# Optimization experiments

Hardware: AMD Instinct MI355X
Metric: run time of the kernel (lower is better)

## Reference

```python
import jax, jax.numpy as jnp
import numpy as np

NUM_QUERIES = 900
EMBED_DIM = 256
NUM_HEADS = 8
EPS = 1e-5


def bilinear_sample(feats, grid):
    """F.grid_sample(..., align_corners=False, padding_mode='zeros', bilinear).
    feats: [BN, C, H, W], grid: [BN, Q, 2] in [-1,1] (x, y). Returns [BN, Q, C]."""
    BN, C, H, W = feats.shape
    ix = (grid[..., 0] + 1.0) * (W * 0.5) - 0.5
    iy = (grid[..., 1] + 1.0) * (H * 0.5) - 0.5
    x0 = jnp.floor(ix)
    y0 = jnp.floor(iy)
    wx1 = ix - x0
    wy1 = iy - y0
    x0i = x0.astype(jnp.int32)
    y0i = y0.astype(jnp.int32)
    x1i = x0i + 1
    y1i = y0i + 1
    b = jnp.arange(BN)[:, None]

    def gather(yy, xx):
        inb = (xx >= 0) & (xx < W) & (yy >= 0) & (yy < H)
        yc = jnp.clip(yy, 0, H - 1)
        xc = jnp.clip(xx, 0, W - 1)
        v = feats[b, :, yc, xc]  # [BN, Q, C]
        return v * inb[..., None].astype(feats.dtype)

    out = (gather(y0i, x0i) * ((1 - wx1) * (1 - wy1))[..., None]
           + gather(y0i, x1i) * (wx1 * (1 - wy1))[..., None]
           + gather(y1i, x0i) * ((1 - wx1) * wy1)[..., None]
           + gather(y1i, x1i) * (wx1 * wy1)[..., None])
    return out


def setup_inputs() -> dict:
    key = jax.random.key(0)
    ks = jax.random.split(key, 16)
    B, N, C, H, W = 2, 6, 256, 116, 200
    Q, D = NUM_QUERIES, EMBED_DIM
    s = 0.02
    return {
        "image_features": jax.random.normal(ks[0], (B, N, C, H, W), jnp.float32),
        "lidar2img": jax.random.normal(ks[1], (B, N, 4, 4), jnp.float32),
        "query_embedding": jax.random.normal(ks[2], (Q, D), jnp.float32) * s,
        "ref_w": jax.random.normal(ks[3], (3, D), jnp.float32) * s,
        "ref_b": jnp.zeros((3,), jnp.float32),
        "in_proj_w": jax.random.normal(ks[4], (3 * D, D), jnp.float32) * s,
        "in_proj_b": jnp.zeros((3 * D,), jnp.float32),
        "out_proj_w": jax.random.normal(ks[5], (D, D), jnp.float32) * s,
        "out_proj_b": jnp.zeros((D,), jnp.float32),
        "norm_w": jnp.ones((D,), jnp.float32),
        "norm_b": jnp.zeros((D,), jnp.float32),
        "cls_w": jax.random.normal(ks[6], (2, D), jnp.float32) * s,
        "cls_b": jnp.zeros((2,), jnp.float32),
        "box_w": jax.random.normal(ks[7], (6, D), jnp.float32) * s,
        "box_b": jnp.zeros((6,), jnp.float32),
    }


def reference(image_features, lidar2img, query_embedding, ref_w, ref_b,
              in_proj_w, in_proj_b, out_proj_w, out_proj_b,
              norm_w, norm_b, cls_w, cls_b, box_w, box_b):
    B, N, C, H, W = image_features.shape
    Q, D = query_embedding.shape

    q = jnp.broadcast_to(query_embedding[None], (B, Q, D))

    # reference points in [0,1]^3
    ref = jax.nn.sigmoid(q @ ref_w.T + ref_b)  # [B,Q,3]

    # 3D -> 2D projection per camera
    homo = jnp.concatenate([ref, jnp.ones_like(ref[..., :1])], axis=-1)  # [B,Q,4]
    p2h = jnp.einsum('bnij,bqj->bnqi', lidar2img, homo)  # [B,N,Q,4]
    z = p2h[..., 2:3]
    pts2d = p2h[..., 0:2] / (jnp.abs(z) + 1e-5)  # [B,N,Q,2]
    mask = (z > 1e-5)[..., 0]  # [B,N,Q]

    # normalize to [-1,1]
    pn = jnp.stack([pts2d[..., 0] / (W - 1) * 2 - 1,
                    pts2d[..., 1] / (H - 1) * 2 - 1], axis=-1)  # [B,N,Q,2]

    feats_flat = image_features.reshape(B * N, C, H, W)
    grid = pn.reshape(B * N, Q, 2)
    sampled = bilinear_sample(feats_flat, grid)            # [BN,Q,C]
    sampled = sampled.reshape(B, N, Q, C).transpose(0, 2, 1, 3)  # [B,Q,N,C]

    mask_t = mask.transpose(0, 2, 1)[..., None]  # [B,Q,N,1]
    # faithful to torch .view(B,Q,N,2): a raw row-major reshape, not a transpose
    pn_view = pn.reshape(B, Q, N, 2)
    valid = mask_t & (jnp.max(jnp.abs(pn_view), axis=-1, keepdims=True) < 1)  # [B,Q,N,1]
    validf = valid.astype(sampled.dtype)

    sum_feats = jnp.sum(sampled * validf, axis=2)  # [B,Q,C]
    count = jnp.clip(jnp.sum(validf, axis=2), 1.0, None)
    tgt = sum_feats / count

    x = q + tgt  # [B,Q,D]

    # MultiheadAttention (batch_first, 8 heads, no dropout)
    qkv = x @ in_proj_w.T + in_proj_b
    qh, kh, vh = jnp.split(qkv, 3, axis=-1)
    hd = D // NUM_HEADS
    def heads(t):
        return t.reshape(B, Q, NUM_HEADS, hd).transpose(0, 2, 1, 3)  # [B,h,Q,hd]
    qh, kh, vh = heads(qh), heads(kh), heads(vh)
    scores = jnp.einsum('bhqd,bhkd->bhqk', qh, kh) / jnp.sqrt(jnp.asarray(hd, x.dtype))
    attn = jax.nn.softmax(scores, axis=-1)
    o = jnp.einsum('bhqk,bhkd->bhqd', attn, vh).transpose(0, 2, 1, 3).reshape(B, Q, D)
    o = o @ out_proj_w.T + out_proj_b

    # LayerNorm (no residual, faithful to the module)
    mu = jnp.mean(o, axis=-1, keepdims=True)
    var = jnp.mean((o - mu) ** 2, axis=-1, keepdims=True)
    xn = (o - mu) / jnp.sqrt(var + EPS) * norm_w + norm_b

    box = xn @ box_w.T + box_b
    box = jnp.concatenate([jax.nn.sigmoid(box[..., :3]), box[..., 3:]], axis=-1)
    cls = xn @ cls_w.T + cls_b
    return cls, box
```

## Files before the change

kernel.cpp:

```cpp
#include <hip/hip_runtime.h>
#include <math.h>

#define BB 2
#define NCAM 6
#define CC 256
#define HH 116
#define WW 200
#define QQ 900
#define DD 256
#define NHD 8
#define HD 32
#define HWSZ (HH*WW)

__device__ __forceinline__ float sigmoidf_(float x){ return 1.0f/(1.0f+expf(-x)); }

__global__ void ref_kernel(const float* __restrict__ qe, const float* __restrict__ ref_w,
                           const float* __restrict__ ref_b, float* __restrict__ ref) {
    int idx = blockIdx.x*256 + threadIdx.x;
    if (idx >= QQ*3) return;
    int q = idx/3, j = idx%3;
    float acc = ref_b[j];
    const float4* qr = (const float4*)(qe + q*DD);
    const float4* wr = (const float4*)(ref_w + j*DD);
    for (int k=0;k<DD/4;k++) {
        float4 a = qr[k], w = wr[k];
        acc += a.x*w.x + a.y*w.y + a.z*w.z + a.w*w.w;
    }
    ref[idx] = sigmoidf_(acc);
}

__global__ void proj_kernel(const float* __restrict__ l2i, const float* __restrict__ ref,
        float* __restrict__ wxa, float* __restrict__ wya,
        int* __restrict__ x0a, int* __restrict__ y0a,
        int* __restrict__ maskz, int* __restrict__ inimg) {
    int idx = blockIdx.x*256+threadIdx.x;
    if (idx >= BB*NCAM*QQ) return;
    int q = idx % QQ;
    int bn = idx / QQ;
    float h0 = ref[q*3+0], h1 = ref[q*3+1], h2 = ref[q*3+2];
    const float* m = l2i + bn*16;
    float px = m[0]*h0+m[1]*h1+m[2]*h2+m[3];
    float py = m[4]*h0+m[5]*h1+m[6]*h2+m[7];
    float pz = m[8]*h0+m[9]*h1+m[10]*h2+m[11];
    float denom = fabsf(pz)+1e-5f;
    float sx = px/denom, sy = py/denom;
    float pnx = sx/(float)(WW-1)*2.0f-1.0f;
    float pny = sy/(float)(HH-1)*2.0f-1.0f;
    maskz[idx] = (pz > 1e-5f) ? 1 : 0;
    inimg[idx] = (fmaxf(fabsf(pnx),fabsf(pny)) < 1.0f) ? 1 : 0;
    float ix = (pnx+1.0f)*(WW*0.5f)-0.5f;
    float iy = (pny+1.0f)*(HH*0.5f)-0.5f;
    float x0f = floorf(ix), y0f = floorf(iy);
    wxa[idx] = ix-x0f; wya[idx] = iy-y0f;
    x0a[idx] = (int)x0f; y0a[idx] = (int)y0f;
}

__global__ __launch_bounds__(256) void sample_kernel(const float* __restrict__ feats,
        const float* __restrict__ qe, const float* __restrict__ wxa, const float* __restrict__ wya,
        const int* __restrict__ x0a, const int* __restrict__ y0a,
        const int* __restrict__ maskz, const int* __restrict__ inimg,
        float* __restrict__ xout) {
    int bq = blockIdx.x;
    int b = bq / QQ, q = bq % QQ;
    int c = threadIdx.x;
    float sum = 0.0f;
    int cnt = 0;
    #pragma unroll
    for (int n = 0; n < NCAM; n++) {
        int s = (b*NCAM+n)*QQ + q;
        int sq = b*(NCAM*QQ) + q*NCAM + n;
        int v = maskz[s] & inimg[sq];
        if (!v) continue;
        cnt++;
        float wx = wxa[s], wy = wya[s];
        int x0 = x0a[s], y0 = y0a[s];
        int x1 = x0 + 1, y1 = y0 + 1;
        bool x0in = (unsigned)x0 < (unsigned)WW;
        bool x1in = (unsigned)x1 < (unsigned)WW;
        bool y0in = (unsigned)y0 < (unsigned)HH;
        bool y1in = (unsigned)y1 < (unsigned)HH;
        int x0c = x0in ? x0 : 0;
        int x1c = x1in ? x1 : (WW-1);
        int y0c = y0in ? y0 : 0;
        int y1c = y1in ? y1 : (HH-1);
        float w00 = (x0in && y0in) ? (1.f-wx)*(1.f-wy) : 0.f;
        float w10 = (x1in && y0in) ? wx*(1.f-wy) : 0.f;
        float w01 = (x0in && y1in) ? (1.f-wx)*wy : 0.f;
        float w11 = (x1in && y1in) ? wx*wy : 0.f;
        const float* fb = feats + ((size_t)(b*NCAM+n)*CC + c)*HWSZ;
        const float* r0 = fb + y0c*WW;
        const float* r1 = fb + y1c*WW;
        sum += w00*r0[x0c] + w10*r0[x1c] + w01*r1[x0c] + w11*r1[x1c];
    }
    float tgt = sum / (float)(cnt > 0 ? cnt : 1);
    xout[(size_t)bq*DD + c] = qe[q*DD+c] + tgt;
}

#define TILE 64
#define BKK 16
__global__ __launch_bounds__(256) void sgemm_nt(const float* __restrict__ A,
        const float* __restrict__ Bw, const float* __restrict__ bias,
        float* __restrict__ Cm, int M, int N, int K) {
    __shared__ float As[BKK][TILE+4];
    __shared__ float Bs[BKK][TILE+4];
    int tid = threadIdx.x;
    int m0 = blockIdx.y * TILE, n0 = blockIdx.x * TILE;
    float acc[4][4] = {};
    int tx = tid & 15, ty = tid >> 4;
    int ms = tid >> 2;
    int kq = (tid & 3) * 4;
    for (int k0 = 0; k0 < K; k0 += BKK) {
        int gm = m0 + ms;
        float4 fa = (gm < M) ? *(const float4*)(A + (size_t)gm * K + k0 + kq)
                             : make_float4(0.f,0.f,0.f,0.f);
        As[kq+0][ms]=fa.x; As[kq+1][ms]=fa.y; As[kq+2][ms]=fa.z; As[kq+3][ms]=fa.w;
        int gn = n0 + ms;
        float4 fb = (gn < N) ? *(const float4*)(Bw + (size_t)gn * K + k0 + kq)
                             : make_float4(0.f,0.f,0.f,0.f);
        Bs[kq+0][ms]=fb.x; Bs[kq+1][ms]=fb.y; Bs[kq+2][ms]=fb.z; Bs[kq+3][ms]=fb.w;
        __syncthreads();
        #pragma unroll
        for (int k = 0; k < BKK; k++) {
            float a[4], bb[4];
            #pragma unroll
            for (int i = 0; i < 4; i++) a[i] = As[k][ty*4+i];
            #pragma unroll
            for (int j = 0; j < 4; j++) bb[j] = Bs[k][tx*4+j];
            #pragma unroll
            for (int i = 0; i < 4; i++)
                #pragma unroll
                for (int j = 0; j < 4; j++)
                    acc[i][j] += a[i] * bb[j];
        }
        __syncthreads();
    }
    for (int i = 0; i < 4; i++) {
        int gm = m0 + ty*4 + i;
        if (gm >= M) continue;
        for (int j = 0; j < 4; j++) {
            int gn = n0 + tx*4 + j;
            if (gn < N) Cm[(size_t)gm * N + gn] = acc[i][j] + bias[gn];
        }
    }
}

#define QTILE 32
#define KTILE 64
#define NQB 29
__global__ __launch_bounds__(256) void attn_flash(const float* __restrict__ qkv,
        float* __restrict__ opA, float* __restrict__ opB,
        float* __restrict__ lpA, float* __restrict__ lpB) {
    __shared__ __align__(16) float Ks[32][68];
    __shared__ __align__(16) float Vs[64][36];
    __shared__ __align__(16) float Ps[32][68];
    int blk = blockIdx.x;
    int qb = blk % NQB;
    int h  = (blk / NQB) % NHD;
    int b  = (blk / (NQB*NHD)) % BB;
    int ks = blk / (NQB*NHD*BB);
    int q0 = qb * QTILE;
    int tid = threadIdx.x;
    int tx = tid & 15, ty = tid >> 4;

    {
        int q = tid >> 3;
        int dseg = (tid & 7) * 4;
        int gq = q0 + q; if (gq > QQ-1) gq = QQ-1;
        const float4 f = *(const float4*)(qkv + ((size_t)(b*QQ+gq))*768 + h*HD + dseg);
        Ps[dseg+0][q] = f.x; Ps[dseg+1][q] = f.y; Ps[dseg+2][q] = f.z; Ps[dseg+3][q] = f.w;
    }
    __syncthreads();
    float q0r[32], q1r[32];
    #pragma unroll
    for (int d = 0; d < 32; d++) { q0r[d] = Ps[d][ty*2]; q1r[d] = Ps[d][ty*2+1]; }
    __syncthreads();

    float O[2][2] = {};
    float l[2] = {0.f, 0.f};
    const float scale = 0.17677669529663689f;
    int kt0 = ks ? 8 : 0;
    int kt1 = ks ? 15 : 8;

    for (int kt = kt0; kt < kt1; kt++) {
        int k0 = kt * KTILE;
        {
            int k = tid >> 2;
            int dseg = (tid & 3) * 8;
            int gk = k0 + k; if (gk > QQ-1) gk = QQ-1;
            const float* kp = qkv + ((size_t)(b*QQ+gk))*768 + 256 + h*HD + dseg;
            float4 f0 = *(const float4*)(kp);
            float4 f1 = *(const float4*)(kp+4);
            Ks[dseg+0][k]=f0.x; Ks[dseg+1][k]=f0.y; Ks[dseg+2][k]=f0.z; Ks[dseg+3][k]=f0.w;
            Ks[dseg+4][k]=f1.x; Ks[dseg+5][k]=f1.y; Ks[dseg+6][k]=f1.z; Ks[dseg+7][k]=f1.w;
            const float* vp = qkv + ((size_t)(b*QQ+gk))*768 + 512 + h*HD + dseg;
            *(float4*)(&Vs[k][dseg])   = *(const float4*)(vp);
            *(float4*)(&Vs[k][dseg+4]) = *(const float4*)(vp+4);
        }
        __syncthreads();

        float acc[2][4] = {};
        #pragma unroll
        for (int d = 0; d < 32; d++) {
            float4 bk = *(const float4*)(&Ks[d][tx*4]);
            float a0 = q0r[d], a1 = q1r[d];
            acc[0][0] += a0*bk.x; acc[0][1] += a0*bk.y; acc[0][2] += a0*bk.z; acc[0][3] += a0*bk.w;
            acc[1][0] += a1*bk.x; acc[1][1] += a1*bk.y; acc[1][2] += a1*bk.z; acc[1][3] += a1*bk.w;
        }
        #pragma unroll
        for (int i = 0; i < 2; i++) {
            float e[4];
            float rs = 0.f;
            #pragma unroll
            for (int j = 0; j < 4; j++) {
                int gk = k0 + tx*4 + j;
                float v = (gk < QQ) ? __expf(acc[i][j]*scale) : 0.f;
                e[j] = v; rs += v;
            }
            #pragma unroll
            for (int m = 1; m < 16; m <<= 1) rs += __shfl_xor(rs, m, 16);
            l[i] += rs;
            *(float4*)(&Ps[ty*2+i][tx*4]) = make_float4(e[0],e[1],e[2],e[3]);
        }
        __syncthreads();

        #pragma unroll
        for (int k4 = 0; k4 < 16; k4++) {
            float4 p0 = *(const float4*)(&Ps[ty*2][k4*4]);
            float4 p1 = *(const float4*)(&Ps[ty*2+1][k4*4]);
            float2 v0 = *(const float2*)(&Vs[k4*4+0][tx*2]);
            float2 v1 = *(const float2*)(&Vs[k4*4+1][tx*2]);
            float2 v2 = *(const float2*)(&Vs[k4*4+2][tx*2]);
            float2 v3 = *(const float2*)(&Vs[k4*4+3][tx*2]);
            O[0][0] += p0.x*v0.x + p0.y*v1.x + p0.z*v2.x + p0.w*v3.x;
            O[0][1] += p0.x*v0.y + p0.y*v1.y + p0.z*v2.y + p0.w*v3.y;
            O[1][0] += p1.x*v0.x + p1.y*v1.x + p1.z*v2.x + p1.w*v3.x;
            O[1][1] += p1.x*v0.y + p1.y*v1.y + p1.z*v2.y + p1.w*v3.y;
        }
        __syncthreads();
    }

    float* op = ks ? opB : opA;
    float* lp = ks ? lpB : lpA;
    #pragma unroll
    for (int i = 0; i < 2; i++) {
        int gq = q0 + ty*2 + i;
        if (gq < QQ) {
            float* o = op + (((size_t)(b*NHD+h))*QQ + gq)*HD + tx*2;
            o[0] = O[i][0];
            o[1] = O[i][1];
            if (tx == 0) lp[(b*NHD+h)*QQ + gq] = l[i];
        }
    }
}

__global__ __launch_bounds__(256) void attn_combine(const float* __restrict__ opA,
        const float* __restrict__ opB, const float* __restrict__ lpA,
        const float* __restrict__ lpB, float* __restrict__ attn_out) {
    int idx = blockIdx.x*256 + threadIdx.x;
    if (idx >= BB*QQ*DD) return;
    int c = idx & 255;
    int bq = idx >> 8;
    int b = bq / QQ, q = bq % QQ;
    int h = c >> 5, d = c & 31;
    size_t base = ((size_t)(b*NHD+h))*QQ + q;
    float o = opA[base*HD + d] + opB[base*HD + d];
    float L = lpA[base] + lpB[base];
    attn_out[idx] = o / L;
}

__global__ __launch_bounds__(256) void final_kernel(const float* __restrict__ o,
    const float* __restrict__ norm_w, const float* __restrict__ norm_b,
    const float* __restrict__ cls_w, const float* __restrict__ cls_b,
    const float* __restrict__ box_w, const float* __restrict__ box_b,
    float* __restrict__ out) {
    __shared__ float s_xn[DD];
    __shared__ float red[8];
    int bq = blockIdx.x;
    int t = threadIdx.x;
    float val = o[(size_t)bq*DD + t];
    float v1 = val, v2 = val*val;
    for (int off=32; off>0; off>>=1) { v1 += __shfl_down(v1, off); v2 += __shfl_down(v2, off); }
    if ((t & 63) == 0) { red[t>>6] = v1; red[4 + (t>>6)] = v2; }
    __syncthreads();
    float ssum = red[0]+red[1]+red[2]+red[3];
    float ssq  = red[4]+red[5]+red[6]+red[7];
    float mu = ssum / (float)DD;
    float var = ssq / (float)DD - mu*mu;
    float inv = 1.0f / sqrtf(var + 1e-5f);
    s_xn[t] = (val - mu)*inv*norm_w[t] + norm_b[t];
    __syncthreads();
    int j = t >> 5, lane = t & 31;
    const float* wrow = (j < 2) ? (cls_w + j*DD) : (box_w + (j-2)*DD);
    float acc = 0.f;
    for (int k=lane; k<DD; k+=32) acc += s_xn[k]*wrow[k];
    for (int off=16; off>0; off>>=1) acc += __shfl_down(acc, off, 32);
    if (lane == 0) {
        if (j < 2) {
            out[(size_t)bq*2 + j] = acc + cls_b[j];
        } else {
            int jj = j-2;
            float v = acc + box_b[jj];
            if (jj < 3) v = sigmoidf_(v);
            out[BB*QQ*2 + (size_t)bq*6 + jj] = v;
        }
    }
}

extern "C" void kernel_launch(void* const* d_in, const int* in_sizes, int n_in,
                              void* d_out, int out_size, void* d_ws, size_t ws_size,
                              hipStream_t stream) {
    const float* feats = (const float*)d_in[0];
    const float* l2i   = (const float*)d_in[1];
    const float* qe    = (const float*)d_in[2];
    const float* ref_w = (const float*)d_in[3];
    const float* ref_b = (const float*)d_in[4];
    const float* ipw   = (const float*)d_in[5];
    const float* ipb   = (const float*)d_in[6];
    const float* opw   = (const float*)d_in[7];
    const float* opb   = (const float*)d_in[8];
    const float* nw    = (const float*)d_in[9];
    const float* nb    = (const float*)d_in[10];
    const float* clsw  = (const float*)d_in[11];
    const float* clsb  = (const float*)d_in[12];
    const float* boxw  = (const float*)d_in[13];
    const float* boxb  = (const float*)d_in[14];
    float* out = (float*)d_out;
    float* ws = (float*)d_ws;

    float* ref   = ws;
    float* wxa   = ws + 2700;
    float* wya   = wxa + 10800;
    int*   x0a   = (int*)(wya + 10800);
    int*   y0a   = x0a + 10800;
    int*   maskz = y0a + 10800;
    int*   inimg = maskz + 10800;
    float* x     = (float*)(inimg + 10800);
    float* qkv   = x + 460800;
    float* attn  = qkv + 1382400;
    float* oproj = attn + 460800;

    float* opA = x;
    float* opB = oproj;
    float* lpA = wxa;
    float* lpB = wxa + 14400;

    ref_kernel<<<(QQ*3+255)/256, 256, 0, stream>>>(qe, ref_w, ref_b, ref);
    proj_kernel<<<(BB*NCAM*QQ+255)/256, 256, 0, stream>>>(l2i, ref, wxa, wya, x0a, y0a, maskz, inimg);
    sample_kernel<<<BB*QQ, 256, 0, stream>>>(feats, qe, wxa, wya, x0a, y0a, maskz, inimg, x);
    sgemm_nt<<<dim3(768/TILE, (BB*QQ+TILE-1)/TILE), 256, 0, stream>>>(x, ipw, ipb, qkv, BB*QQ, 768, 256);
    attn_flash<<<BB*NHD*NQB*2, 256, 0, stream>>>(qkv, opA, opB, lpA, lpB);
    attn_combine<<<(BB*QQ*DD+255)/256, 256, 0, stream>>>(opA, opB, lpA, lpB, attn);
    sgemm_nt<<<dim3(256/TILE, (BB*QQ+TILE-1)/TILE), 256, 0, stream>>>(attn, opw, opb, oproj, BB*QQ, 256, 256);
    final_kernel<<<BB*QQ, 256, 0, stream>>>(oproj, nw, nb, clsw, clsb, boxw, boxb, out);
}
```

Before: 469.7 us.

## Fuse ref projection into proj, batch sampler loads, fold attn combine into GEMM

The ref-point linear plus sigmoid is computed inside proj_kernel, so ref_kernel is gone. sample_kernel stages the per-camera sampling parameters in shared memory and issues all bilinear gathers before reducing, which exposes more memory-level parallelism. The split-K attention combine (sum the partials and divide by L) is folded into the output-projection GEMM's A-tile load, removing a kernel launch and an intermediate buffer round trip. The cost is redundant ref dot products (once per camera and batch) and a heavier A-load path in the GEMM.

```diff
diff --git a/kernel.cpp b/kernel.cpp
--- a/kernel.cpp
+++ b/kernel.cpp
@@ -14,22 +14,8 @@
 
 __device__ __forceinline__ float sigmoidf_(float x){ return 1.0f/(1.0f+expf(-x)); }
 
-__global__ void ref_kernel(const float* __restrict__ qe, const float* __restrict__ ref_w,
-                           const float* __restrict__ ref_b, float* __restrict__ ref) {
-    int idx = blockIdx.x*256 + threadIdx.x;
-    if (idx >= QQ*3) return;
-    int q = idx/3, j = idx%3;
-    float acc = ref_b[j];
-    const float4* qr = (const float4*)(qe + q*DD);
-    const float4* wr = (const float4*)(ref_w + j*DD);
-    for (int k=0;k<DD/4;k++) {
-        float4 a = qr[k], w = wr[k];
-        acc += a.x*w.x + a.y*w.y + a.z*w.z + a.w*w.w;
-    }
-    ref[idx] = sigmoidf_(acc);
-}
-
-__global__ void proj_kernel(const float* __restrict__ l2i, const float* __restrict__ ref,
+__global__ void proj_kernel(const float* __restrict__ l2i, const float* __restrict__ qe,
+        const float* __restrict__ ref_w, const float* __restrict__ ref_b,
         float* __restrict__ wxa, float* __restrict__ wya,
         int* __restrict__ x0a, int* __restrict__ y0a,
         int* __restrict__ maskz, int* __restrict__ inimg) {
@@ -37,7 +23,20 @@
     if (idx >= BB*NCAM*QQ) return;
     int q = idx % QQ;
     int bn = idx / QQ;
-    float h0 = ref[q*3+0], h1 = ref[q*3+1], h2 = ref[q*3+2];
+    float a0 = ref_b[0], a1 = ref_b[1], a2 = ref_b[2];
+    const float4* qr = (const float4*)(qe + (size_t)q*DD);
+    const float4* w0 = (const float4*)(ref_w);
+    const float4* w1 = (const float4*)(ref_w + DD);
+    const float4* w2 = (const float4*)(ref_w + 2*DD);
+    #pragma unroll 4
+    for (int k=0;k<DD/4;k++) {
+        float4 a = qr[k];
+        float4 b0 = w0[k], b1 = w1[k], b2 = w2[k];
+        a0 += a.x*b0.x + a.y*b0.y + a.z*b0.z + a.w*b0.w;
+        a1 += a.x*b1.x + a.y*b1.y + a.z*b1.z + a.w*b1.w;
+        a2 += a.x*b2.x + a.y*b2.y + a.z*b2.z + a.w*b2.w;
+    }
+    float h0 = sigmoidf_(a0), h1 = sigmoidf_(a1), h2 = sigmoidf_(a2);
     const float* m = l2i + bn*16;
     float px = m[0]*h0+m[1]*h1+m[2]*h2+m[3];
     float py = m[4]*h0+m[5]*h1+m[6]*h2+m[7];
@@ -60,20 +59,29 @@
         const int* __restrict__ x0a, const int* __restrict__ y0a,
         const int* __restrict__ maskz, const int* __restrict__ inimg,
         float* __restrict__ xout) {
+    __shared__ float swx[NCAM], swy[NCAM];
+    __shared__ int sx0[NCAM], sy0[NCAM], sval[NCAM];
     int bq = blockIdx.x;
     int b = bq / QQ, q = bq % QQ;
-    int c = threadIdx.x;
-    float sum = 0.0f;
+    int t = threadIdx.x;
+    if (t < NCAM) {
+        int n = t;
+        int s = (b*NCAM+n)*QQ + q;
+        int sq = b*(NCAM*QQ) + q*NCAM + n;
+        sval[n] = maskz[s] & inimg[sq];
+        swx[n] = wxa[s]; swy[n] = wya[s];
+        sx0[n] = x0a[s]; sy0[n] = y0a[s];
+    }
+    __syncthreads();
+    int c = t;
+    float v00[NCAM] = {}, v10[NCAM] = {}, v01[NCAM] = {}, v11[NCAM] = {};
+    float W00[NCAM], W10[NCAM], W01[NCAM], W11[NCAM];
     int cnt = 0;
     #pragma unroll
     for (int n = 0; n < NCAM; n++) {
-        int s = (b*NCAM+n)*QQ + q;
-        int sq = b*(NCAM*QQ) + q*NCAM + n;
-        int v = maskz[s] & inimg[sq];
-        if (!v) continue;
-        cnt++;
-        float wx = wxa[s], wy = wya[s];
-        int x0 = x0a[s], y0 = y0a[s];
+        int valid = sval[n];
+        float wx = swx[n], wy = swy[n];
+        int x0 = sx0[n], y0 = sy0[n];
         int x1 = x0 + 1, y1 = y0 + 1;
         bool x0in = (unsigned)x0 < (unsigned)WW;
         bool x1in = (unsigned)x1 < (unsigned)WW;
@@ -83,22 +91,32 @@
         int x1c = x1in ? x1 : (WW-1);
         int y0c = y0in ? y0 : 0;
         int y1c = y1in ? y1 : (HH-1);
-        float w00 = (x0in && y0in) ? (1.f-wx)*(1.f-wy) : 0.f;
-        float w10 = (x1in && y0in) ? wx*(1.f-wy) : 0.f;
-        float w01 = (x0in && y1in) ? (1.f-wx)*wy : 0.f;
-        float w11 = (x1in && y1in) ? wx*wy : 0.f;
-        const float* fb = feats + ((size_t)(b*NCAM+n)*CC + c)*HWSZ;
-        const float* r0 = fb + y0c*WW;
-        const float* r1 = fb + y1c*WW;
-        sum += w00*r0[x0c] + w10*r0[x1c] + w01*r1[x0c] + w11*r1[x1c];
-    }
+        W00[n] = (x0in && y0in) ? (1.f-wx)*(1.f-wy) : 0.f;
+        W10[n] = (x1in && y0in) ? wx*(1.f-wy) : 0.f;
+        W01[n] = (x0in && y1in) ? (1.f-wx)*wy : 0.f;
+        W11[n] = (x1in && y1in) ? wx*wy : 0.f;
+        cnt += valid;
+        if (valid) {
+            const float* fb = feats + ((size_t)(b*NCAM+n)*CC + c)*HWSZ;
+            const float* r0 = fb + y0c*WW;
+            const float* r1 = fb + y1c*WW;
+            v00[n] = r0[x0c]; v10[n] = r0[x1c];
+            v01[n] = r1[x0c]; v11[n] = r1[x1c];
+        }
+    }
+    float sum = 0.0f;
+    #pragma unroll
+    for (int n = 0; n < NCAM; n++)
+        sum += W00[n]*v00[n] + W10[n]*v10[n] + W01[n]*v01[n] + W11[n]*v11[n];
     float tgt = sum / (float)(cnt > 0 ? cnt : 1);
     xout[(size_t)bq*DD + c] = qe[q*DD+c] + tgt;
 }
 
 #define TILE 64
 #define BKK 16
+template<bool COMB>
 __global__ __launch_bounds__(256) void sgemm_nt(const float* __restrict__ A,
+        const float* __restrict__ A2, const float* __restrict__ lA, const float* __restrict__ lB,
         const float* __restrict__ Bw, const float* __restrict__ bias,
         float* __restrict__ Cm, int M, int N, int K) {
     __shared__ float As[BKK][TILE+4];
@@ -111,8 +129,23 @@
     int kq = (tid & 3) * 4;
     for (int k0 = 0; k0 < K; k0 += BKK) {
         int gm = m0 + ms;
-        float4 fa = (gm < M) ? *(const float4*)(A + (size_t)gm * K + k0 + kq)
-                             : make_float4(0.f,0.f,0.f,0.f);
+        float4 fa = make_float4(0.f,0.f,0.f,0.f);
+        if (gm < M) {
+            if (COMB) {
+                int k = k0 + kq;
+                int h = k >> 5, d = k & 31;
+                int b = (gm >= QQ) ? 1 : 0;
+                int qq_ = gm - b*QQ;
+                size_t base = ((size_t)(b*NHD+h))*QQ + qq_;
+                const float4 o1 = *(const float4*)(A  + base*HD + d);
+                const float4 o2 = *(const float4*)(A2 + base*HD + d);
+                float L = lA[base] + lB[base];
+                float r = 1.0f / L;
+                fa = make_float4((o1.x+o2.x)*r, (o1.y+o2.y)*r, (o1.z+o2.z)*r, (o1.w+o2.w)*r);
+            } else {
+                fa = *(const float4*)(A + (size_t)gm * K + k0 + kq);
+            }
+        }
         As[kq+0][ms]=fa.x; As[kq+1][ms]=fa.y; As[kq+2][ms]=fa.z; As[kq+3][ms]=fa.w;
         int gn = n0 + ms;
         float4 fb = (gn < N) ? *(const float4*)(Bw + (size_t)gn * K + k0 + kq)
@@ -251,21 +284,6 @@
             if (tx == 0) lp[(b*NHD+h)*QQ + gq] = l[i];
         }
     }
-}
-
-__global__ __launch_bounds__(256) void attn_combine(const float* __restrict__ opA,
-        const float* __restrict__ opB, const float* __restrict__ lpA,
-        const float* __restrict__ lpB, float* __restrict__ attn_out) {
-    int idx = blockIdx.x*256 + threadIdx.x;
-    if (idx >= BB*QQ*DD) return;
-    int c = idx & 255;
-    int bq = idx >> 8;
-    int b = bq / QQ, q = bq % QQ;
-    int h = c >> 5, d = c & 31;
-    size_t base = ((size_t)(b*NHD+h))*QQ + q;
-    float o = opA[base*HD + d] + opB[base*HD + d];
-    float L = lpA[base] + lpB[base];
-    attn_out[idx] = o / L;
 }
 
 __global__ __launch_bounds__(256) void final_kernel(const float* __restrict__ o,
@@ -338,18 +356,20 @@
     float* qkv   = x + 460800;
     float* attn  = qkv + 1382400;
     float* oproj = attn + 460800;
+    (void)ref;
 
     float* opA = x;
-    float* opB = oproj;
+    float* opB = attn;
     float* lpA = wxa;
     float* lpB = wxa + 14400;
 
-    ref_kernel<<<(QQ*3+255)/256, 256, 0, stream>>>(qe, ref_w, ref_b, ref);
-    proj_kernel<<<(BB*NCAM*QQ+255)/256, 256, 0, stream>>>(l2i, ref, wxa, wya, x0a, y0a, maskz, inimg);
+    proj_kernel<<<(BB*NCAM*QQ+255)/256, 256, 0, stream>>>(l2i, qe, ref_w, ref_b,
+                                                          wxa, wya, x0a, y0a, maskz, inimg);
     sample_kernel<<<BB*QQ, 256, 0, stream>>>(feats, qe, wxa, wya, x0a, y0a, maskz, inimg, x);
-    sgemm_nt<<<dim3(768/TILE, (BB*QQ+TILE-1)/TILE), 256, 0, stream>>>(x, ipw, ipb, qkv, BB*QQ, 768, 256);
+    sgemm_nt<false><<<dim3(768/TILE, (BB*QQ+TILE-1)/TILE), 256, 0, stream>>>(
+        x, nullptr, nullptr, nullptr, ipw, ipb, qkv, BB*QQ, 768, 256);
     attn_flash<<<BB*NHD*NQB*2, 256, 0, stream>>>(qkv, opA, opB, lpA, lpB);
-    attn_combine<<<(BB*QQ*DD+255)/256, 256, 0, stream>>>(opA, opB, lpA, lpB, attn);
-    sgemm_nt<<<dim3(256/TILE, (BB*QQ+TILE-1)/TILE), 256, 0, stream>>>(attn, opw, opb, oproj, BB*QQ, 256, 256);
+    sgemm_nt<true><<<dim3(256/TILE, (BB*QQ+TILE-1)/TILE), 256, 0, stream>>>(
+        opA, opB, lpA, lpB, opw, opb, oproj, BB*QQ, 256, 256);
     final_kernel<<<BB*QQ, 256, 0, stream>>>(oproj, nw, nb, clsw, clsb, boxw, boxb, out);
 }
```

After: 466.1 us. Within noise of the previous version (-0.8%).
